# Kernel optimization log

Measured on AMD Instinct MI355X. Metric: run time of the kernel, lower is better.

Reference implementation:

```python
import jax, jax.numpy as jnp
import numpy as np

N = 50000
F_IN = 512
H1 = 500
H2 = 100
C = 16
E = 800000


def setup_inputs() -> dict:
    key = jax.random.key(0)
    ks = jax.random.split(key, 8)
    x = jax.random.normal(ks[0], (N, F_IN), dtype=jnp.float32)
    edge_index = jax.random.randint(ks[1], (2, E), 0, N, dtype=jnp.int64)
    W1 = jax.random.normal(ks[2], (F_IN, H1), dtype=jnp.float32) / np.sqrt(F_IN)
    b1 = jnp.zeros((H1,), dtype=jnp.float32)
    W2 = jax.random.normal(ks[3], (H1, H2), dtype=jnp.float32) / np.sqrt(H1)
    b2 = jnp.zeros((H2,), dtype=jnp.float32)
    W3 = jax.random.normal(ks[4], (H2, C), dtype=jnp.float32) / np.sqrt(H2)
    b3 = jnp.zeros((C,), dtype=jnp.float32)
    return {"x": x, "edge_index": edge_index, "W1": W1, "b1": b1,
            "W2": W2, "b2": b2, "W3": W3, "b3": b3}


def _edge_norm(edge_index, num_nodes):
    # add self loops (as in torch add_self_loops), then symmetric degree norm
    loops = jnp.arange(num_nodes, dtype=edge_index.dtype)
    row = jnp.concatenate([edge_index[0], loops])
    col = jnp.concatenate([edge_index[1], loops])
    deg = jax.ops.segment_sum(jnp.ones_like(row, dtype=jnp.float32), row,
                              num_segments=num_nodes)
    dinv = jnp.where(deg > 0, deg ** -0.5, 0.0)  # norm[isinf] = 0
    norm = dinv[row] * dinv[col]
    return row, col, norm


def _graph_conv(x, row, col, norm, W, b, num_nodes):
    h = x @ W + b                                  # [N, out]
    msg = norm[:, None] * h[col]                   # gather + scale, [E', out]
    return jax.ops.segment_sum(msg, row, num_segments=num_nodes)  # SpMM


def reference(x, edge_index, W1, b1, W2, b2, W3, b3):
    num_nodes = x.shape[0]
    row, col, norm = _edge_norm(edge_index, num_nodes)
    h = jnp.tanh(_graph_conv(x, row, col, norm, W1, b1, num_nodes))
    h = jnp.tanh(_graph_conv(h, row, col, norm, W2, b2, num_nodes))
    h = jnp.tanh(_graph_conv(h, row, col, norm, W3, b3, num_nodes))
    return jax.nn.softmax(h, axis=1)
```

## Files before the change

kernel.cpp:

```cpp
#include <hip/hip_runtime.h>
#include <math.h>

#define NN  50000
#define FIN 512
#define HH1 500
#define HH2 100
#define NC  16
#define NE  800000
#define KD  512
#define LDP 40

typedef __attribute__((ext_vector_type(4))) float    f32x4;
typedef __attribute__((ext_vector_type(4))) _Float16 f16x4;
typedef __attribute__((ext_vector_type(8))) _Float16 f16x8;
typedef __attribute__((ext_vector_type(8))) unsigned short u16x8;


__global__ void zero2_k(int* a, int* b) {
    int i = blockIdx.x * blockDim.x + threadIdx.x;
    if (i < NN) { a[i] = 0; b[i] = 0; }
}

__global__ void hist_k(const int* __restrict__ rows, int* __restrict__ rowcnt) {
    int i = blockIdx.x * blockDim.x + threadIdx.x;
    if (i < NE) atomicAdd(&rowcnt[rows[i]], 1);
}

__global__ void dinv_k(const int* __restrict__ rowcnt, float* __restrict__ dinv) {
    int i = blockIdx.x * blockDim.x + threadIdx.x;
    if (i < NN) dinv[i] = rsqrtf((float)(rowcnt[i] + 1));
}

__global__ __launch_bounds__(1024) void scan_k(const int* __restrict__ cnt,
                                               int* __restrict__ ptr) {
    __shared__ int s[1024];
    __shared__ int carry;
    int t = threadIdx.x;
    if (t == 0) carry = 0;
    __syncthreads();
    for (int base = 0; base < NN; base += 1024) {
        int i = base + t;
        int v = (i < NN) ? cnt[i] : 0;
        s[t] = v;
        __syncthreads();
        #pragma unroll
        for (int off = 1; off < 1024; off <<= 1) {
            int add = (t >= off) ? s[t - off] : 0;
            __syncthreads();
            s[t] += add;
            __syncthreads();
        }
        int excl = s[t] - v;
        if (i < NN) ptr[i] = carry + excl;
        __syncthreads();
        if (t == 1023) carry += s[1023];
        __syncthreads();
    }
}

__global__ void scatter_k(const int* __restrict__ rows, const int* __restrict__ cols,
                          const float* __restrict__ dinv,
                          const int* __restrict__ row_ptr, int* __restrict__ fill,
                          int* __restrict__ col_s, float* __restrict__ w_s) {
    int e = blockIdx.x * blockDim.x + threadIdx.x;
    if (e >= NE) return;
    int r = rows[e], c = cols[e];
    int pos = row_ptr[r] + atomicAdd(&fill[r], 1);
    col_s[pos] = c;
    w_s[pos] = dinv[r] * dinv[c];
}


__global__ void wconv_k(const float* __restrict__ W, _Float16* __restrict__ Wt,
                        int k, int m)
{
    int idx = blockIdx.x * 256 + threadIdx.x;
    int n_ = idx >> 9;
    int kk = idx & 511;
    float v = (kk < k && n_ < m) ? W[(size_t)kk * m + n_] : 0.0f;
    Wt[idx] = (_Float16)v;
}


template<int AF16>
__global__ __launch_bounds__(256) void gemm_f16_k(
    const void* __restrict__ Av, const _Float16* __restrict__ Wt,
    const float* __restrict__ bias, _Float16* __restrict__ Cb,
    int mpad, int n, int m)
{
    __shared__ __align__(16) _Float16 As[128 * LDP];
    __shared__ __align__(16) _Float16 Bs[128 * LDP];

    const float*    Af32 = (const float*)Av;
    const _Float16* Af16 = (const _Float16*)Av;

    int tid  = threadIdx.x;
    int lane = tid & 63;
    int wid  = tid >> 6;
    int wrow = wid & 1, wcol = wid >> 1;
    int lr = lane & 15, q = lane >> 4;
    int row0 = blockIdx.x * 128, col0 = blockIdx.y * 128;

    f32x4 acc[4][4];
    #pragma unroll
    for (int i = 0; i < 4; i++)
        #pragma unroll
        for (int j = 0; j < 4; j++) acc[i][j] = (f32x4){0.f, 0.f, 0.f, 0.f};

    float4 pa32[4];
    u16x8  pa16[2];
    u16x8  pb[2];

    auto load_pf = [&](int kt) {
        if (AF16 == 0) {
            #pragma unroll
            for (int i = 0; i < 4; i++) {
                int idx = tid + i * 256;
                int rr = idx >> 3, c4 = idx & 7;
                int gr = row0 + rr;
                pa32[i] = (gr < n) ? *(const float4*)(Af32 + (size_t)gr * KD + kt + c4 * 4)
                                   : make_float4(0.f, 0.f, 0.f, 0.f);
            }
        } else {
            #pragma unroll
            for (int i = 0; i < 2; i++) {
                int idx = tid + i * 256;
                int rr = idx >> 2, c8 = idx & 3;
                int gr = row0 + rr;
                pa16[i] = (gr < n) ? *(const u16x8*)(Af16 + (size_t)gr * KD + kt + c8 * 8)
                                   : (u16x8){0, 0, 0, 0, 0, 0, 0, 0};
            }
        }
        #pragma unroll
        for (int i = 0; i < 2; i++) {
            int idx = tid + i * 256;
            int rr = idx >> 2, c8 = idx & 3;
            pb[i] = *(const u16x8*)(Wt + (size_t)(col0 + rr) * KD + kt + c8 * 8);
        }
    };

    load_pf(0);

    for (int step = 0; step < KD / 32; step++) {
        __syncthreads();
        if (AF16 == 0) {
            #pragma unroll
            for (int i = 0; i < 4; i++) {
                int idx = tid + i * 256;
                int rr = idx >> 3, c4 = idx & 7;
                float4 v = pa32[i];
                f16x4 hv = {(_Float16)v.x, (_Float16)v.y, (_Float16)v.z, (_Float16)v.w};
                *(f16x4*)(As + rr * LDP + c4 * 4) = hv;
            }
        } else {
            #pragma unroll
            for (int i = 0; i < 2; i++) {
                int idx = tid + i * 256;
                int rr = idx >> 2, c8 = idx & 3;
                *(u16x8*)(As + rr * LDP + c8 * 8) = pa16[i];
            }
        }
        #pragma unroll
        for (int i = 0; i < 2; i++) {
            int idx = tid + i * 256;
            int rr = idx >> 2, c8 = idx & 3;
            *(u16x8*)(Bs + rr * LDP + c8 * 8) = pb[i];
        }
        __syncthreads();

        if (step + 1 < KD / 32) load_pf((step + 1) * 32);

        f16x8 a[4], b[4];
        #pragma unroll
        for (int t = 0; t < 4; t++) {
            a[t] = *(const f16x8*)(As + (wrow * 64 + t * 16 + lr) * LDP + q * 8);
            b[t] = *(const f16x8*)(Bs + (wcol * 64 + t * 16 + lr) * LDP + q * 8);
        }
        #pragma unroll
        for (int ti = 0; ti < 4; ti++)
            #pragma unroll
            for (int tj = 0; tj < 4; tj++)
                acc[ti][tj] = __builtin_amdgcn_mfma_f32_16x16x32_f16(
                    a[ti], b[tj], acc[ti][tj], 0, 0, 0);
    }

    #pragma unroll
    for (int ti = 0; ti < 4; ti++) {
        #pragma unroll
        for (int tj = 0; tj < 4; tj++) {
            int col = col0 + wcol * 64 + tj * 16 + lr;
            if (col >= mpad) continue;
            bool valid = col < m;
            float bv = valid ? bias[col] : 0.0f;
            #pragma unroll
            for (int p = 0; p < 4; p++) {
                int row = row0 + wrow * 64 + ti * 16 + q * 4 + p;
                if (row < n) {
                    float v = valid ? (acc[ti][tj][p] + bv) : 0.0f;
                    Cb[(size_t)row * mpad + col] = (_Float16)v;
                }
            }
        }
    }
}


#define BM 64
#define BN 64
#define BK 16

__global__ __launch_bounds__(256) void gemm_bias_k(
    const float* __restrict__ A, const float* __restrict__ W,
    const float* __restrict__ bias, float* __restrict__ C,
    int n, int k, int m)
{
    __shared__ float As[BK][BM + 1];
    __shared__ float Ws[BK][BN];

    int tid = threadIdx.x;
    int tx = tid & 15;
    int ty = tid >> 4;
    int row0 = blockIdx.x * BM;
    int col0 = blockIdx.y * BN;

    float acc[4][4] = {};

    for (int kt = 0; kt < k; kt += BK) {
        #pragma unroll
        for (int i = 0; i < 4; i++) {
            int idx = tid + i * 256;
            int r  = idx >> 4;
            int kk = idx & 15;
            int gr = row0 + r, gk = kt + kk;
            As[kk][r] = (gr < n && gk < k) ? A[(size_t)gr * k + gk] : 0.0f;
        }
        #pragma unroll
        for (int i = 0; i < 4; i++) {
            int idx = tid + i * 256;
            int kk = idx >> 6;
            int c  = idx & 63;
            int gk = kt + kk, gc = col0 + c;
            Ws[kk][c] = (gk < k && gc < m) ? W[(size_t)gk * m + gc] : 0.0f;
        }
        __syncthreads();

        #pragma unroll
        for (int kk = 0; kk < BK; kk++) {
            float a[4], w[4];
            #pragma unroll
            for (int i = 0; i < 4; i++) a[i] = As[kk][ty * 4 + i];
            #pragma unroll
            for (int j = 0; j < 4; j++) w[j] = Ws[kk][tx * 4 + j];
            #pragma unroll
            for (int i = 0; i < 4; i++)
                #pragma unroll
                for (int j = 0; j < 4; j++)
                    acc[i][j] += a[i] * w[j];
        }
        __syncthreads();
    }

    #pragma unroll
    for (int i = 0; i < 4; i++) {
        int gr = row0 + ty * 4 + i;
        if (gr >= n) continue;
        #pragma unroll
        for (int j = 0; j < 4; j++) {
            int gc = col0 + tx * 4 + j;
            if (gc < m) C[(size_t)gr * m + gc] = acc[i][j] + bias[gc];
        }
    }
}


__device__ __forceinline__ float h2f(unsigned short u) {
    union { unsigned short s; _Float16 f; } t; t.s = u; return (float)t.f;
}

__device__ __forceinline__ void fma_h8(f32x4& a0, f32x4& a1, u16x8 v, float w) {
    #pragma unroll
    for (int i = 0; i < 4; i++) a0[i] += w * h2f(v[i]);
    #pragma unroll
    for (int i = 0; i < 4; i++) a1[i] += w * h2f(v[4 + i]);
}


__global__ __launch_bounds__(256) void spmm_f16_500_k(
    const int* __restrict__ row_ptr, const int* __restrict__ rowcnt,
    const int* __restrict__ col_s, const float* __restrict__ w_s,
    const float* __restrict__ dinv, const _Float16* __restrict__ hb,
    _Float16* __restrict__ outh)
{
    int r = blockIdx.x * 4 + (threadIdx.x >> 6);
    int lane = threadIdx.x & 63;
    if (r >= NN) return;

    const u16x8* h8 = (const u16x8*)hb;

    float d = dinv[r];
    f32x4 acc0 = {0.f, 0.f, 0.f, 0.f}, acc1 = {0.f, 0.f, 0.f, 0.f};
    fma_h8(acc0, acc1, h8[(size_t)r * 64 + lane], d * d);

    int beg = row_ptr[r], cnt = rowcnt[r];
    int j = 0;
    for (; j + 3 < cnt; j += 4) {
        int   c0 = col_s[beg + j],     c1 = col_s[beg + j + 1];
        int   c2 = col_s[beg + j + 2], c3 = col_s[beg + j + 3];
        float w0 = w_s[beg + j],       w1 = w_s[beg + j + 1];
        float w2 = w_s[beg + j + 2],   w3 = w_s[beg + j + 3];
        u16x8 v0 = h8[(size_t)c0 * 64 + lane];
        u16x8 v1 = h8[(size_t)c1 * 64 + lane];
        u16x8 v2 = h8[(size_t)c2 * 64 + lane];
        u16x8 v3 = h8[(size_t)c3 * 64 + lane];
        fma_h8(acc0, acc1, v0, w0);
        fma_h8(acc0, acc1, v1, w1);
        fma_h8(acc0, acc1, v2, w2);
        fma_h8(acc0, acc1, v3, w3);
    }
    for (; j < cnt; j++) {
        fma_h8(acc0, acc1, h8[(size_t)col_s[beg + j] * 64 + lane], w_s[beg + j]);
    }

    int f0 = lane * 8;
    f16x8 o;
    #pragma unroll
    for (int i = 0; i < 4; i++)
        o[i] = (_Float16)((f0 + i < HH1) ? tanhf(acc0[i]) : 0.0f);
    #pragma unroll
    for (int i = 0; i < 4; i++)
        o[4 + i] = (_Float16)((f0 + 4 + i < HH1) ? tanhf(acc1[i]) : 0.0f);
    __builtin_nontemporal_store(o, (f16x8*)(outh + (size_t)r * KD + f0));
}


__global__ __launch_bounds__(256) void spmm_f16_100_k(
    const int* __restrict__ row_ptr, const int* __restrict__ rowcnt,
    const int* __restrict__ col_s, const float* __restrict__ w_s,
    const float* __restrict__ dinv, const _Float16* __restrict__ hb,
    float* __restrict__ out)
{
    int r = blockIdx.x * 16 + (threadIdx.x >> 4);
    int lane = threadIdx.x & 15;
    if (r >= NN) return;

    const u16x8* h8 = (const u16x8*)hb;

    float d = dinv[r];
    f32x4 acc0 = {0.f, 0.f, 0.f, 0.f}, acc1 = {0.f, 0.f, 0.f, 0.f};
    fma_h8(acc0, acc1, h8[(size_t)r * 16 + lane], d * d);

    int beg = row_ptr[r], cnt = rowcnt[r];
    int j = 0;
    for (; j + 3 < cnt; j += 4) {
        int   c0 = col_s[beg + j],     c1 = col_s[beg + j + 1];
        int   c2 = col_s[beg + j + 2], c3 = col_s[beg + j + 3];
        float w0 = w_s[beg + j],       w1 = w_s[beg + j + 1];
        float w2 = w_s[beg + j + 2],   w3 = w_s[beg + j + 3];
        u16x8 v0 = h8[(size_t)c0 * 16 + lane];
        u16x8 v1 = h8[(size_t)c1 * 16 + lane];
        u16x8 v2 = h8[(size_t)c2 * 16 + lane];
        u16x8 v3 = h8[(size_t)c3 * 16 + lane];
        fma_h8(acc0, acc1, v0, w0);
        fma_h8(acc0, acc1, v1, w1);
        fma_h8(acc0, acc1, v2, w2);
        fma_h8(acc0, acc1, v3, w3);
    }
    for (; j < cnt; j++) {
        fma_h8(acc0, acc1, h8[(size_t)col_s[beg + j] * 16 + lane], w_s[beg + j]);
    }

    int f0 = lane * 8;
    f32x4 t0, t1;
    #pragma unroll
    for (int i = 0; i < 4; i++) { t0[i] = tanhf(acc0[i]); t1[i] = tanhf(acc1[i]); }
    if (f0 + 4 <= HH2)
        __builtin_nontemporal_store(t0, (f32x4*)(out + (size_t)r * HH2 + f0));
    if (f0 + 8 <= HH2)
        __builtin_nontemporal_store(t1, (f32x4*)(out + (size_t)r * HH2 + f0 + 4));
}


template<int TPR, int NV, int ACT>
__global__ __launch_bounds__(256) void spmm_csr_k(
    const int* __restrict__ row_ptr, const int* __restrict__ rowcnt,
    const int* __restrict__ col_s, const float* __restrict__ w_s,
    const float* __restrict__ dinv, const float* __restrict__ h,
    float* __restrict__ out)
{
    const int rpb = 256 / TPR;
    int r = blockIdx.x * rpb + threadIdx.x / TPR;
    int lane = threadIdx.x % TPR;
    if (r >= NN) return;
    bool active = lane < NV;

    const f32x4* h4 = (const f32x4*)h;
    f32x4* o4 = (f32x4*)out;

    float d = dinv[r];
    f32x4 acc = {0.f, 0.f, 0.f, 0.f};
    if (active) acc = (d * d) * h4[(size_t)r * NV + lane];

    int beg = row_ptr[r], cnt = rowcnt[r];
    int j = 0;
    for (; j + 3 < cnt; j += 4) {
        int   c0 = col_s[beg + j],     c1 = col_s[beg + j + 1];
        int   c2 = col_s[beg + j + 2], c3 = col_s[beg + j + 3];
        float w0 = w_s[beg + j],       w1 = w_s[beg + j + 1];
        float w2 = w_s[beg + j + 2],   w3 = w_s[beg + j + 3];
        if (active) {
            f32x4 v0 = h4[(size_t)c0 * NV + lane];
            f32x4 v1 = h4[(size_t)c1 * NV + lane];
            f32x4 v2 = h4[(size_t)c2 * NV + lane];
            f32x4 v3 = h4[(size_t)c3 * NV + lane];
            acc += w0 * v0; acc += w1 * v1; acc += w2 * v2; acc += w3 * v3;
        }
    }
    for (; j < cnt; j++) {
        int   c0 = col_s[beg + j];
        float w0 = w_s[beg + j];
        if (active) acc += w0 * h4[(size_t)c0 * NV + lane];
    }

    if (active) {
        if (ACT == 1) {
            acc.x = tanhf(acc.x); acc.y = tanhf(acc.y);
            acc.z = tanhf(acc.z); acc.w = tanhf(acc.w);
        }
        __builtin_nontemporal_store(acc, &o4[(size_t)r * NV + lane]);
    }
}

__global__ void tanh_softmax_k(const float* __restrict__ in, float* __restrict__ out) {
    int r = blockIdx.x * blockDim.x + threadIdx.x;
    if (r >= NN) return;
    float v[NC];
    float mx = -1e30f;
    #pragma unroll
    for (int j = 0; j < NC; j++) {
        v[j] = tanhf(in[r * NC + j]);
        mx = fmaxf(mx, v[j]);
    }
    float s = 0.0f;
    #pragma unroll
    for (int j = 0; j < NC; j++) { v[j] = expf(v[j] - mx); s += v[j]; }
    float inv = 1.0f / s;
    #pragma unroll
    for (int j = 0; j < NC; j++) out[r * NC + j] = v[j] * inv;
}


extern "C" void kernel_launch(void* const* d_in, const int* in_sizes, int n_in,
                              void* d_out, int out_size, void* d_ws, size_t ws_size,
                              hipStream_t stream)
{
    const float* x  = (const float*)d_in[0];
    const int*   ei = (const int*)d_in[1];
    const float* W1 = (const float*)d_in[2];
    const float* b1 = (const float*)d_in[3];
    const float* W2 = (const float*)d_in[4];
    const float* b2 = (const float*)d_in[5];
    const float* W3 = (const float*)d_in[6];
    const float* b3 = (const float*)d_in[7];
    float* out = (float*)d_out;

    const int* rows = ei;
    const int* cols = ei + NE;

    char* p = (char*)d_ws;
    float*     dinv    = (float*)p;     p += (size_t)NN * 4;
    int*       rowcnt  = (int*)p;       p += (size_t)NN * 4;
    int*       row_ptr = (int*)p;       p += (size_t)NN * 4;
    int*       fill    = (int*)p;       p += (size_t)NN * 4;
    int*       col_s   = (int*)p;       p += (size_t)NE * 4;
    float*     w_s     = (float*)p;     p += (size_t)NE * 4;
    float*     h2      = (float*)p;     p += (size_t)NN * HH2 * 4;
    float*     A3      = (float*)p;     p += (size_t)NN * NC * 4;
    float*     B3      = (float*)p;     p += (size_t)NN * NC * 4;
    _Float16*  A1h     = (_Float16*)p;  p += (size_t)NN * KD * 2;
    _Float16*  h1h     = (_Float16*)p;  p += (size_t)NN * KD * 2;
    _Float16*  A2h     = (_Float16*)p;  p += (size_t)NN * 128 * 2;
    _Float16*  Wt1     = (_Float16*)p;  p += (size_t)512 * KD * 2;
    _Float16*  Wt2     = (_Float16*)p;  p += (size_t)128 * KD * 2;

    const int T = 256;

    zero2_k<<<(NN + T - 1) / T, T, 0, stream>>>(rowcnt, fill);
    hist_k<<<(NE + T - 1) / T, T, 0, stream>>>(rows, rowcnt);
    dinv_k<<<(NN + T - 1) / T, T, 0, stream>>>(rowcnt, dinv);
    scan_k<<<1, 1024, 0, stream>>>(rowcnt, row_ptr);
    scatter_k<<<(NE + T - 1) / T, T, 0, stream>>>(rows, cols, dinv, row_ptr, fill,
                                                  col_s, w_s);
    wconv_k<<<512 * KD / 256, T, 0, stream>>>(W1, Wt1, FIN, HH1);
    wconv_k<<<128 * KD / 256, T, 0, stream>>>(W2, Wt2, HH1, HH2);

    {
        dim3 g((NN + 127) / 128, 4);
        gemm_f16_k<0><<<g, T, 0, stream>>>(x, Wt1, b1, A1h, KD, NN, HH1);
        spmm_f16_500_k<<<(NN + 3) / 4, T, 0, stream>>>(row_ptr, rowcnt, col_s, w_s,
                                                       dinv, A1h, h1h);
    }
    {
        dim3 g((NN + 127) / 128, 1);
        gemm_f16_k<1><<<g, T, 0, stream>>>(h1h, Wt2, b2, A2h, 128, NN, HH2);
        spmm_f16_100_k<<<(NN + 15) / 16, T, 0, stream>>>(row_ptr, rowcnt, col_s, w_s,
                                                         dinv, A2h, h2);
    }
    {
        dim3 g((NN + BM - 1) / BM, (NC + BN - 1) / BN);
        gemm_bias_k<<<g, T, 0, stream>>>(h2, W3, b3, A3, NN, HH2, NC);
        spmm_csr_k<4, 4, 0><<<(NN + 63) / 64, T, 0, stream>>>(
            row_ptr, rowcnt, col_s, w_s, dinv, A3, B3);
        tanh_softmax_k<<<(NN + T - 1) / T, T, 0, stream>>>(B3, out);
    }
}
```

Measured before the change: 643.8 us.

## Move layer-3 to fp16 MFMA GEMM, parallelize scan, merge weight conversions

Replaces the single-block serial prefix scan with a three-kernel multi-block scan. The three weight conversions are merged into one launch. Layer 2 now writes fp16 h2 padded to 128 columns, and layer 3 uses the fp16 MFMA GEMM (K=128) and an fp16-gather SpMM in place of the fp32 SIMT GEMM and fp32 SpMM. The aim is to remove the serial scan latency, shrink the bytes moved in layer 3 and use the matrix cores, at the cost of more launches and reduced precision in the last layer.

```diff
diff --git a/kernel.cpp b/kernel.cpp
--- a/kernel.cpp
+++ b/kernel.cpp
@@ -31,31 +31,42 @@
     if (i < NN) dinv[i] = rsqrtf((float)(rowcnt[i] + 1));
 }
 
-__global__ __launch_bounds__(1024) void scan_k(const int* __restrict__ cnt,
-                                               int* __restrict__ ptr) {
+__global__ __launch_bounds__(1024) void scan1_k(const int* __restrict__ cnt,
+                                                int* __restrict__ excl,
+                                                int* __restrict__ bsum) {
     __shared__ int s[1024];
-    __shared__ int carry;
     int t = threadIdx.x;
-    if (t == 0) carry = 0;
+    int i = blockIdx.x * 1024 + t;
+    int v = (i < NN) ? cnt[i] : 0;
+    s[t] = v;
     __syncthreads();
-    for (int base = 0; base < NN; base += 1024) {
-        int i = base + t;
-        int v = (i < NN) ? cnt[i] : 0;
-        s[t] = v;
+    #pragma unroll
+    for (int off = 1; off < 1024; off <<= 1) {
+        int add = (t >= off) ? s[t - off] : 0;
         __syncthreads();
-        #pragma unroll
-        for (int off = 1; off < 1024; off <<= 1) {
-            int add = (t >= off) ? s[t - off] : 0;
-            __syncthreads();
-            s[t] += add;
-            __syncthreads();
-        }
-        int excl = s[t] - v;
-        if (i < NN) ptr[i] = carry + excl;
+        s[t] += add;
         __syncthreads();
-        if (t == 1023) carry += s[1023];
-        __syncthreads();
-    }
+    }
+    if (i < NN) excl[i] = s[t] - v;
+    if (t == 1023) bsum[blockIdx.x] = s[1023];
+}
+
+__global__ void scan2_k(int* bsum, int nb) {
+    int lane = threadIdx.x;
+    int orig = (lane < nb) ? bsum[lane] : 0;
+    int v = orig;
+    #pragma unroll
+    for (int off = 1; off < 64; off <<= 1) {
+        int u = __shfl_up(v, off, 64);
+        if (lane >= off) v += u;
+    }
+    if (lane < nb) bsum[lane] = v - orig;
+}
+
+__global__ void scan3_k(const int* __restrict__ excl, const int* __restrict__ bsum,
+                        int* __restrict__ ptr) {
+    int i = blockIdx.x * 256 + threadIdx.x;
+    if (i < NN) ptr[i] = excl[i] + bsum[i >> 10];
 }
 
 __global__ void scatter_k(const int* __restrict__ rows, const int* __restrict__ cols,
@@ -71,18 +82,34 @@
 }
 
 
-__global__ void wconv_k(const float* __restrict__ W, _Float16* __restrict__ Wt,
-                        int k, int m)
+#define R1 (512 * 512)
+#define R2 (128 * 512)
+#define R3 (128 * 128)
+
+__global__ void wconv3_k(const float* __restrict__ W1, const float* __restrict__ W2,
+                         const float* __restrict__ W3, _Float16* __restrict__ Wt1,
+                         _Float16* __restrict__ Wt2, _Float16* __restrict__ Wt3)
 {
     int idx = blockIdx.x * 256 + threadIdx.x;
-    int n_ = idx >> 9;
-    int kk = idx & 511;
-    float v = (kk < k && n_ < m) ? W[(size_t)kk * m + n_] : 0.0f;
-    Wt[idx] = (_Float16)v;
-}
-
-
-template<int AF16>
+    if (idx < R1) {
+        int n_ = idx >> 9, kk = idx & 511;
+        float v = (n_ < HH1) ? W1[(size_t)kk * HH1 + n_] : 0.0f;
+        Wt1[idx] = (_Float16)v;
+    } else if (idx < R1 + R2) {
+        int j = idx - R1;
+        int n_ = j >> 9, kk = j & 511;
+        float v = (kk < HH1 && n_ < HH2) ? W2[(size_t)kk * HH2 + n_] : 0.0f;
+        Wt2[j] = (_Float16)v;
+    } else if (idx < R1 + R2 + R3) {
+        int j = idx - R1 - R2;
+        int n_ = j >> 7, kk = j & 127;
+        float v = (kk < HH2 && n_ < NC) ? W3[(size_t)kk * NC + n_] : 0.0f;
+        Wt3[j] = (_Float16)v;
+    }
+}
+
+
+template<int AF16, int KDIM>
 __global__ __launch_bounds__(256) void gemm_f16_k(
     const void* __restrict__ Av, const _Float16* __restrict__ Wt,
     const float* __restrict__ bias, _Float16* __restrict__ Cb,
@@ -118,7 +145,7 @@
                 int idx = tid + i * 256;
                 int rr = idx >> 3, c4 = idx & 7;
                 int gr = row0 + rr;
-                pa32[i] = (gr < n) ? *(const float4*)(Af32 + (size_t)gr * KD + kt + c4 * 4)
+                pa32[i] = (gr < n) ? *(const float4*)(Af32 + (size_t)gr * KDIM + kt + c4 * 4)
                                    : make_float4(0.f, 0.f, 0.f, 0.f);
             }
         } else {
@@ -127,7 +154,7 @@
                 int idx = tid + i * 256;
                 int rr = idx >> 2, c8 = idx & 3;
                 int gr = row0 + rr;
-                pa16[i] = (gr < n) ? *(const u16x8*)(Af16 + (size_t)gr * KD + kt + c8 * 8)
+                pa16[i] = (gr < n) ? *(const u16x8*)(Af16 + (size_t)gr * KDIM + kt + c8 * 8)
                                    : (u16x8){0, 0, 0, 0, 0, 0, 0, 0};
             }
         }
@@ -135,13 +162,13 @@
         for (int i = 0; i < 2; i++) {
             int idx = tid + i * 256;
             int rr = idx >> 2, c8 = idx & 3;
-            pb[i] = *(const u16x8*)(Wt + (size_t)(col0 + rr) * KD + kt + c8 * 8);
+            pb[i] = *(const u16x8*)(Wt + (size_t)(col0 + rr) * KDIM + kt + c8 * 8);
         }
     };
 
     load_pf(0);
 
-    for (int step = 0; step < KD / 32; step++) {
+    for (int step = 0; step < KDIM / 32; step++) {
         __syncthreads();
         if (AF16 == 0) {
             #pragma unroll
@@ -168,7 +195,7 @@
         }
         __syncthreads();
 
-        if (step + 1 < KD / 32) load_pf((step + 1) * 32);
+        if (step + 1 < KDIM / 32) load_pf((step + 1) * 32);
 
         f16x8 a[4], b[4];
         #pragma unroll
@@ -200,74 +227,6 @@
                     Cb[(size_t)row * mpad + col] = (_Float16)v;
                 }
             }
-        }
-    }
-}
-
-
-#define BM 64
-#define BN 64
-#define BK 16
-
-__global__ __launch_bounds__(256) void gemm_bias_k(
-    const float* __restrict__ A, const float* __restrict__ W,
-    const float* __restrict__ bias, float* __restrict__ C,
-    int n, int k, int m)
-{
-    __shared__ float As[BK][BM + 1];
-    __shared__ float Ws[BK][BN];
-
-    int tid = threadIdx.x;
-    int tx = tid & 15;
-    int ty = tid >> 4;
-    int row0 = blockIdx.x * BM;
-    int col0 = blockIdx.y * BN;
-
-    float acc[4][4] = {};
-
-    for (int kt = 0; kt < k; kt += BK) {
-        #pragma unroll
-        for (int i = 0; i < 4; i++) {
-            int idx = tid + i * 256;
-            int r  = idx >> 4;
-            int kk = idx & 15;
-            int gr = row0 + r, gk = kt + kk;
-            As[kk][r] = (gr < n && gk < k) ? A[(size_t)gr * k + gk] : 0.0f;
-        }
-        #pragma unroll
-        for (int i = 0; i < 4; i++) {
-            int idx = tid + i * 256;
-            int kk = idx >> 6;
-            int c  = idx & 63;
-            int gk = kt + kk, gc = col0 + c;
-            Ws[kk][c] = (gk < k && gc < m) ? W[(size_t)gk * m + gc] : 0.0f;
-        }
-        __syncthreads();
-
-        #pragma unroll
-        for (int kk = 0; kk < BK; kk++) {
-            float a[4], w[4];
-            #pragma unroll
-            for (int i = 0; i < 4; i++) a[i] = As[kk][ty * 4 + i];
-            #pragma unroll
-            for (int j = 0; j < 4; j++) w[j] = Ws[kk][tx * 4 + j];
-            #pragma unroll
-            for (int i = 0; i < 4; i++)
-                #pragma unroll
-                for (int j = 0; j < 4; j++)
-                    acc[i][j] += a[i] * w[j];
-        }
-        __syncthreads();
-    }
-
-    #pragma unroll
-    for (int i = 0; i < 4; i++) {
-        int gr = row0 + ty * 4 + i;
-        if (gr >= n) continue;
-        #pragma unroll
-        for (int j = 0; j < 4; j++) {
-            int gc = col0 + tx * 4 + j;
-            if (gc < m) C[(size_t)gr * m + gc] = acc[i][j] + bias[gc];
         }
     }
 }
@@ -337,7 +296,7 @@
     const int* __restrict__ row_ptr, const int* __restrict__ rowcnt,
     const int* __restrict__ col_s, const float* __restrict__ w_s,
     const float* __restrict__ dinv, const _Float16* __restrict__ hb,
-    float* __restrict__ out)
+    _Float16* __restrict__ outh)
 {
     int r = blockIdx.x * 16 + (threadIdx.x >> 4);
     int lane = threadIdx.x & 15;
@@ -370,35 +329,32 @@
     }
 
     int f0 = lane * 8;
-    f32x4 t0, t1;
-    #pragma unroll
-    for (int i = 0; i < 4; i++) { t0[i] = tanhf(acc0[i]); t1[i] = tanhf(acc1[i]); }
-    if (f0 + 4 <= HH2)
-        __builtin_nontemporal_store(t0, (f32x4*)(out + (size_t)r * HH2 + f0));
-    if (f0 + 8 <= HH2)
-        __builtin_nontemporal_store(t1, (f32x4*)(out + (size_t)r * HH2 + f0 + 4));
-}
-
-
-template<int TPR, int NV, int ACT>
-__global__ __launch_bounds__(256) void spmm_csr_k(
+    f16x8 o;
+    #pragma unroll
+    for (int i = 0; i < 4; i++)
+        o[i] = (_Float16)((f0 + i < HH2) ? tanhf(acc0[i]) : 0.0f);
+    #pragma unroll
+    for (int i = 0; i < 4; i++)
+        o[4 + i] = (_Float16)((f0 + 4 + i < HH2) ? tanhf(acc1[i]) : 0.0f);
+    __builtin_nontemporal_store(o, (f16x8*)(outh + (size_t)r * 128 + f0));
+}
+
+
+__global__ __launch_bounds__(256) void spmm3h_k(
     const int* __restrict__ row_ptr, const int* __restrict__ rowcnt,
     const int* __restrict__ col_s, const float* __restrict__ w_s,
-    const float* __restrict__ dinv, const float* __restrict__ h,
+    const float* __restrict__ dinv, const _Float16* __restrict__ hb,
     float* __restrict__ out)
 {
-    const int rpb = 256 / TPR;
-    int r = blockIdx.x * rpb + threadIdx.x / TPR;
-    int lane = threadIdx.x % TPR;
+    int r = blockIdx.x * 128 + (threadIdx.x >> 1);
+    int lane = threadIdx.x & 1;
     if (r >= NN) return;
-    bool active = lane < NV;
-
-    const f32x4* h4 = (const f32x4*)h;
-    f32x4* o4 = (f32x4*)out;
+
+    const u16x8* h8 = (const u16x8*)hb;
 
     float d = dinv[r];
-    f32x4 acc = {0.f, 0.f, 0.f, 0.f};
-    if (active) acc = (d * d) * h4[(size_t)r * NV + lane];
+    f32x4 acc0 = {0.f, 0.f, 0.f, 0.f}, acc1 = {0.f, 0.f, 0.f, 0.f};
+    fma_h8(acc0, acc1, h8[(size_t)r * 2 + lane], d * d);
 
     int beg = row_ptr[r], cnt = rowcnt[r];
     int j = 0;
@@ -407,27 +363,22 @@
         int   c2 = col_s[beg + j + 2], c3 = col_s[beg + j + 3];
         float w0 = w_s[beg + j],       w1 = w_s[beg + j + 1];
         float w2 = w_s[beg + j + 2],   w3 = w_s[beg + j + 3];
-        if (active) {
-            f32x4 v0 = h4[(size_t)c0 * NV + lane];
-            f32x4 v1 = h4[(size_t)c1 * NV + lane];
-            f32x4 v2 = h4[(size_t)c2 * NV + lane];
-            f32x4 v3 = h4[(size_t)c3 * NV + lane];
-            acc += w0 * v0; acc += w1 * v1; acc += w2 * v2; acc += w3 * v3;
-        }
+        u16x8 v0 = h8[(size_t)c0 * 2 + lane];
+        u16x8 v1 = h8[(size_t)c1 * 2 + lane];
+        u16x8 v2 = h8[(size_t)c2 * 2 + lane];
+        u16x8 v3 = h8[(size_t)c3 * 2 + lane];
+        fma_h8(acc0, acc1, v0, w0);
+        fma_h8(acc0, acc1, v1, w1);
+        fma_h8(acc0, acc1, v2, w2);
+        fma_h8(acc0, acc1, v3, w3);
     }
     for (; j < cnt; j++) {
-        int   c0 = col_s[beg + j];
-        float w0 = w_s[beg + j];
-        if (active) acc += w0 * h4[(size_t)c0 * NV + lane];
-    }
-
-    if (active) {
-        if (ACT == 1) {
-            acc.x = tanhf(acc.x); acc.y = tanhf(acc.y);
-            acc.z = tanhf(acc.z); acc.w = tanhf(acc.w);
-        }
-        __builtin_nontemporal_store(acc, &o4[(size_t)r * NV + lane]);
-    }
+        fma_h8(acc0, acc1, h8[(size_t)col_s[beg + j] * 2 + lane], w_s[beg + j]);
+    }
+
+    float* o = out + (size_t)r * NC + lane * 8;
+    __builtin_nontemporal_store(acc0, (f32x4*)o);
+    __builtin_nontemporal_store(acc1, (f32x4*)(o + 4));
 }
 
 __global__ void tanh_softmax_k(const float* __restrict__ in, float* __restrict__ out) {
@@ -471,45 +422,50 @@
     int*       rowcnt  = (int*)p;       p += (size_t)NN * 4;
     int*       row_ptr = (int*)p;       p += (size_t)NN * 4;
     int*       fill    = (int*)p;       p += (size_t)NN * 4;
+    int*       excl    = (int*)p;       p += (size_t)NN * 4;
+    int*       bsum    = (int*)p;       p += (size_t)256 * 4;
     int*       col_s   = (int*)p;       p += (size_t)NE * 4;
     float*     w_s     = (float*)p;     p += (size_t)NE * 4;
-    float*     h2      = (float*)p;     p += (size_t)NN * HH2 * 4;
-    float*     A3      = (float*)p;     p += (size_t)NN * NC * 4;
     float*     B3      = (float*)p;     p += (size_t)NN * NC * 4;
     _Float16*  A1h     = (_Float16*)p;  p += (size_t)NN * KD * 2;
     _Float16*  h1h     = (_Float16*)p;  p += (size_t)NN * KD * 2;
     _Float16*  A2h     = (_Float16*)p;  p += (size_t)NN * 128 * 2;
-    _Float16*  Wt1     = (_Float16*)p;  p += (size_t)512 * KD * 2;
-    _Float16*  Wt2     = (_Float16*)p;  p += (size_t)128 * KD * 2;
+    _Float16*  h2h     = (_Float16*)p;  p += (size_t)NN * 128 * 2;
+    _Float16*  A3h     = (_Float16*)p;  p += (size_t)NN * NC * 2;
+    _Float16*  Wt1     = (_Float16*)p;  p += (size_t)R1 * 2;
+    _Float16*  Wt2     = (_Float16*)p;  p += (size_t)R2 * 2;
+    _Float16*  Wt3     = (_Float16*)p;  p += (size_t)R3 * 2;
 
     const int T = 256;
-
+    const int NB = (NN + 1023) / 1024;
+
+    wconv3_k<<<(R1 + R2 + R3) / 256, T, 0, stream>>>(W1, W2, W3, Wt1, Wt2, Wt3);
     zero2_k<<<(NN + T - 1) / T, T, 0, stream>>>(rowcnt, fill);
     hist_k<<<(NE + T - 1) / T, T, 0, stream>>>(rows, rowcnt);
     dinv_k<<<(NN + T - 1) / T, T, 0, stream>>>(rowcnt, dinv);
-    scan_k<<<1, 1024, 0, stream>>>(rowcnt, row_ptr);
+    scan1_k<<<NB, 1024, 0, stream>>>(rowcnt, excl, bsum);
+    scan2_k<<<1, 64, 0, stream>>>(bsum, NB);
+    scan3_k<<<(NN + T - 1) / T, T, 0, stream>>>(excl, bsum, row_ptr);
     scatter_k<<<(NE + T - 1) / T, T, 0, stream>>>(rows, cols, dinv, row_ptr, fill,
                                                   col_s, w_s);
-    wconv_k<<<512 * KD / 256, T, 0, stream>>>(W1, Wt1, FIN, HH1);
-    wconv_k<<<128 * KD / 256, T, 0, stream>>>(W2, Wt2, HH1, HH2);
 
     {
         dim3 g((NN + 127) / 128, 4);
-        gemm_f16_k<0><<<g, T, 0, stream>>>(x, Wt1, b1, A1h, KD, NN, HH1);
+        gemm_f16_k<0, 512><<<g, T, 0, stream>>>(x, Wt1, b1, A1h, KD, NN, HH1);
         spmm_f16_500_k<<<(NN + 3) / 4, T, 0, stream>>>(row_ptr, rowcnt, col_s, w_s,
                                                        dinv, A1h, h1h);
     }
     {
         dim3 g((NN + 127) / 128, 1);
-        gemm_f16_k<1><<<g, T, 0, stream>>>(h1h, Wt2, b2, A2h, 128, NN, HH2);
+        gemm_f16_k<1, 512><<<g, T, 0, stream>>>(h1h, Wt2, b2, A2h, 128, NN, HH2);
         spmm_f16_100_k<<<(NN + 15) / 16, T, 0, stream>>>(row_ptr, rowcnt, col_s, w_s,
-                                                         dinv, A2h, h2);
+                                                         dinv, A2h, h2h);
     }
     {
-        dim3 g((NN + BM - 1) / BM, (NC + BN - 1) / BN);
-        gemm_bias_k<<<g, T, 0, stream>>>(h2, W3, b3, A3, NN, HH2, NC);
-        spmm_csr_k<4, 4, 0><<<(NN + 63) / 64, T, 0, stream>>>(
-            row_ptr, rowcnt, col_s, w_s, dinv, A3, B3);
+        dim3 g((NN + 127) / 128, 1);
+        gemm_f16_k<1, 128><<<g, T, 0, stream>>>(h2h, Wt3, b3, A3h, NC, NN, NC);
+        spmm3h_k<<<(NN + 127) / 128, T, 0, stream>>>(row_ptr, rowcnt, col_s, w_s,
+                                                     dinv, A3h, B3);
         tanh_softmax_k<<<(NN + T - 1) / T, T, 0, stream>>>(B3, out);
     }
 }
```

After: 565.8 us. 12.1% less time.
